# Optimization experiments

Hardware: AMD Instinct MI355X
Metric: run time of the kernel (lower is better)

Reference implementation:

```python
import jax, jax.numpy as jnp
import numpy as np

C = 512
NH = 4
HD = C // NH
G = 32  # min(32, C) and C % 32 == 0
EPS = 1e-5


def setup_inputs() -> dict:
    key = jax.random.key(0)
    ks = jax.random.split(key, 11)
    s = 1.0 / np.sqrt(C)
    return {
        "x": jax.random.normal(ks[0], (16, C, 32, 32), dtype=jnp.float32),
        "gamma": jnp.ones((C,), jnp.float32),
        "beta": jnp.zeros((C,), jnp.float32),
        "wq": jax.random.normal(ks[1], (C, C), jnp.float32) * s,
        "bq": jax.random.normal(ks[2], (C,), jnp.float32) * 0.01,
        "wk": jax.random.normal(ks[3], (C, C), jnp.float32) * s,
        "bk": jax.random.normal(ks[4], (C,), jnp.float32) * 0.01,
        "wv": jax.random.normal(ks[5], (C, C), jnp.float32) * s,
        "bv": jax.random.normal(ks[6], (C,), jnp.float32) * 0.01,
        "wp": jax.random.normal(ks[7], (C, C), jnp.float32) * s,
        "bp": jax.random.normal(ks[8], (C,), jnp.float32) * 0.01,
    }


def _group_norm(x, gamma, beta):
    b, c, h, w = x.shape
    xr = x.reshape(b, G, c // G, h, w)
    mean = xr.mean(axis=(2, 3, 4), keepdims=True)
    var = xr.var(axis=(2, 3, 4), keepdims=True)
    xn = ((xr - mean) * jax.lax.rsqrt(var + EPS)).reshape(b, c, h, w)
    return xn * gamma[None, :, None, None] + beta[None, :, None, None]


def _conv1x1(x, w, b):
    # 1x1 conv == per-position channel GEMM
    return jnp.einsum('oc,bchw->bohw', w, x) + b[None, :, None, None]


def reference(x, gamma, beta, wq, bq, wk, bk, wv, bv, wp, bp):
    b, c, h, w = x.shape
    hw = h * w
    scale = HD ** (-0.5)
    hn = _group_norm(x, gamma, beta)
    q = _conv1x1(hn, wq, bq).reshape(b, NH, HD, hw)
    k = _conv1x1(hn, wk, bk).reshape(b, NH, HD, hw)
    v = _conv1x1(hn, wv, bv).reshape(b, NH, HD, hw)
    attn = jnp.einsum('bhdq,bhdk->bhqk', q, k) * scale  # [b, nh, hw, hw]
    attn = jax.nn.softmax(attn, axis=-1)
    out = jnp.einsum('bhqk,bhdk->bhdq', attn, v)  # [b, nh, hd, hw]
    out = out.reshape(b, c, h, w)
    out = _conv1x1(out, wp, bp)
    return x + out
```

## Files before the change

kernel.cpp:

```cpp
#include <hip/hip_runtime.h>
#include <math.h>

#define CCH 512
#define NH 4
#define HD 128
#define HW 1024
#define BATCH 16
#define EPS 1e-5f

typedef __attribute__((ext_vector_type(8))) short bfrag;
typedef __attribute__((ext_vector_type(4))) float f4;
typedef __attribute__((ext_vector_type(16))) float f16v;

static __device__ __forceinline__ unsigned short f2bf(float f) {
  union { float f; unsigned u; } v;
  v.f = f;
  unsigned r = v.u + 0x7fff + ((v.u >> 16) & 1);
  return (unsigned short)(r >> 16);
}
static __device__ __forceinline__ unsigned pack2(unsigned short a, unsigned short b) {
  return (unsigned)a | ((unsigned)b << 16);
}
static __device__ __forceinline__ unsigned cvt_pk_bf16(float a, float b) {
  unsigned r;
  asm("v_cvt_pk_bf16_f32 %0, %1, %2" : "=v"(r) : "v"(a), "v"(b));
  return r;
}
#if defined(__has_builtin) && __has_builtin(__builtin_amdgcn_exp2f)
#define EXP2(x) __builtin_amdgcn_exp2f(x)
#else
#define EXP2(x) __expf((x) * 0.6931471805599453f)
#endif
static __device__ __forceinline__ void ldg_lds16(const unsigned short* g,
                                                 unsigned short* l) {
  __builtin_amdgcn_global_load_lds(
      (const __attribute__((address_space(1))) unsigned int*)g,
      (__attribute__((address_space(3))) unsigned int*)l, 16, 0, 0);
}

#define QSCALE (0.08838834764831845f * 1.4426950408889634f)

__global__ __launch_bounds__(256) void wcvt_kernel(const float* __restrict__ s0,
                                                   const float* __restrict__ s1,
                                                   const float* __restrict__ s2,
                                                   const float* __restrict__ s3,
                                                   unsigned short* __restrict__ d) {
  const float* srcs[4] = {s0, s1, s2, s3};
  const float* s = srcs[blockIdx.y];
  unsigned short* dp = d + (size_t)blockIdx.y * CCH * CCH;
  int i = blockIdx.x * 256 + threadIdx.x;
  f4 v = ((const f4*)s)[i];
  ushort4 o;
  o.x = f2bf(v.x); o.y = f2bf(v.y); o.z = f2bf(v.z); o.w = f2bf(v.w);
  ((ushort4*)dp)[i] = o;
}

__global__ __launch_bounds__(256) void gn_kernel(const float* __restrict__ x,
                                                 const float* __restrict__ gamma,
                                                 const float* __restrict__ beta,
                                                 unsigned short* __restrict__ hn) {
  int b = blockIdx.x >> 5, g = blockIdx.x & 31;
  const float* xp = x + ((size_t)b * CCH + g * 16) * HW;
  int t = threadIdx.x;
  float s = 0.f, ss = 0.f;
  const f4* xp4 = (const f4*)xp;
  f4 vv[16];
#pragma unroll
  for (int c = 0; c < 16; ++c) {
    f4 v = xp4[c * 256 + t];
    vv[c] = v;
    s += v.x + v.y + v.z + v.w;
    ss += v.x * v.x + v.y * v.y + v.z * v.z + v.w * v.w;
  }
#pragma unroll
  for (int off = 32; off > 0; off >>= 1) {
    s += __shfl_xor(s, off);
    ss += __shfl_xor(ss, off);
  }
  __shared__ float rs[4], rss[4];
  int w = t >> 6;
  if ((t & 63) == 0) { rs[w] = s; rss[w] = ss; }
  __syncthreads();
  s = rs[0] + rs[1] + rs[2] + rs[3];
  ss = rss[0] + rss[1] + rss[2] + rss[3];
  const float invn = 1.f / (16 * HW);
  float mean = s * invn;
  float var = ss * invn - mean * mean;
  float rstd = rsqrtf(var + EPS);
  float a_[16], b_[16];
#pragma unroll
  for (int c = 0; c < 16; ++c) {
    float gm = gamma[g * 16 + c] * rstd;
    a_[c] = gm;
    b_[c] = beta[g * 16 + c] - mean * gm;
  }
#pragma unroll
  for (int i = 0; i < 4; ++i) {
    int p = 4 * t + i;
    uint4 u0, u1;
    u0.x = cvt_pk_bf16(vv[0][i] * a_[0] + b_[0], vv[1][i] * a_[1] + b_[1]);
    u0.y = cvt_pk_bf16(vv[2][i] * a_[2] + b_[2], vv[3][i] * a_[3] + b_[3]);
    u0.z = cvt_pk_bf16(vv[4][i] * a_[4] + b_[4], vv[5][i] * a_[5] + b_[5]);
    u0.w = cvt_pk_bf16(vv[6][i] * a_[6] + b_[6], vv[7][i] * a_[7] + b_[7]);
    u1.x = cvt_pk_bf16(vv[8][i] * a_[8] + b_[8], vv[9][i] * a_[9] + b_[9]);
    u1.y = cvt_pk_bf16(vv[10][i] * a_[10] + b_[10], vv[11][i] * a_[11] + b_[11]);
    u1.z = cvt_pk_bf16(vv[12][i] * a_[12] + b_[12], vv[13][i] * a_[13] + b_[13]);
    u1.w = cvt_pk_bf16(vv[14][i] * a_[14] + b_[14], vv[15][i] * a_[15] + b_[15]);
    unsigned short* dst = hn + ((size_t)b * HW + p) * CCH + g * 16;
    *(uint4*)dst = u0;
    *(uint4*)(dst + 8) = u1;
  }
}

template <int PROJ>
__global__ __launch_bounds__(256, 3) void mm_kernel(
    const unsigned short* __restrict__ Xt, const unsigned short* __restrict__ Wb,
    const float* __restrict__ b0, const float* __restrict__ b1,
    const float* __restrict__ b2, const float* __restrict__ resid,
    unsigned short* __restrict__ O0, unsigned short* __restrict__ O1,
    unsigned short* __restrict__ O2, float* __restrict__ Ofp) {
  int b = blockIdx.z;
  int p0 = blockIdx.x * 128;
  int c0g = blockIdx.y * 128;
  __shared__ __align__(16) unsigned short Xs[2][4096];
  __shared__ __align__(16) unsigned short Ws[2][4096];
  int t = threadIdx.x;
  int w = t >> 6, lane = t & 63, l15 = lane & 15, quad = lane >> 4;
  int wp = (w & 1) * 64, wc = (w >> 1) * 64;
  const unsigned short* Xb = Xt + (size_t)b * HW * CCH;
  const unsigned short* Wr = Wb + (size_t)c0g * CCH;
  f4 acc[4][4] = {};
  auto stage = [&](int k0, int bi) {
#pragma unroll
    for (int j = 0; j < 2; ++j) {
      int chk = w * 2 + j;
      int r = chk * 16 + (lane >> 2);
      int c = (lane & 3) ^ (r & 3);
      ldg_lds16(&Xb[(size_t)(p0 + r) * CCH + k0 + c * 8], &Xs[bi][chk * 512]);
      ldg_lds16(&Wr[(size_t)r * CCH + k0 + c * 8], &Ws[bi][chk * 512]);
    }
  };
  stage(0, 0);
  __syncthreads();
  for (int k0 = 0, cur = 0; k0 < CCH; k0 += 32, cur ^= 1) {
    if (k0 + 32 < CCH) stage(k0 + 32, cur ^ 1);
    bfrag af[4], bf[4];
#pragma unroll
    for (int pt = 0; pt < 4; ++pt) {
      int r = wp + pt * 16 + l15;
      af[pt] = *(const bfrag*)&Xs[cur][r * 32 + (quad ^ (r & 3)) * 8];
    }
#pragma unroll
    for (int ct = 0; ct < 4; ++ct) {
      int r = wc + ct * 16 + l15;
      bf[ct] = *(const bfrag*)&Ws[cur][r * 32 + (quad ^ (r & 3)) * 8];
    }
#pragma unroll
    for (int pt = 0; pt < 4; ++pt)
#pragma unroll
      for (int ct = 0; ct < 4; ++ct)
        acc[pt][ct] = __builtin_amdgcn_mfma_f32_16x16x32_bf16(
            af[pt], bf[ct], acc[pt][ct], 0, 0, 0);
    __syncthreads();
  }
  if (PROJ) {
#pragma unroll
    for (int ct = 0; ct < 4; ++ct) {
      int ch = c0g + wc + ct * 16 + l15;
      float bi = b0[ch];
#pragma unroll
      for (int pt = 0; pt < 4; ++pt) {
        int pos = p0 + wp + pt * 16 + quad * 4;
        f4 v = acc[pt][ct];
        size_t off = (size_t)b * CCH * HW + (size_t)ch * HW + pos;
        float4 rv = *(const float4*)&resid[off];
        float4 st;
        st.x = v.x + bi + rv.x; st.y = v.y + bi + rv.y;
        st.z = v.z + bi + rv.z; st.w = v.w + bi + rv.w;
        *(float4*)&Ofp[off] = st;
      }
    }
  } else {
    int mat = c0g >> 9;
    int c0 = c0g & 511;
    const float* bias = mat == 0 ? b0 : (mat == 1 ? b1 : b2);
    unsigned short* O = mat == 0 ? O0 : (mat == 1 ? O1 : O2);
    const float sc = (mat == 0) ? QSCALE : 1.0f;
#pragma unroll
    for (int ct = 0; ct < 4; ++ct) {
      int ch = c0 + wc + ct * 16 + l15;
      float bi = bias[ch];
#pragma unroll
      for (int pt = 0; pt < 4; ++pt) {
        int pos = p0 + wp + pt * 16 + quad * 4;
        f4 v = acc[pt][ct];
        if (mat < 2) {
          unsigned short* Op = O + (size_t)b * HW * CCH;
          Op[(size_t)(pos + 0) * CCH + ch] = f2bf((v.x + bi) * sc);
          Op[(size_t)(pos + 1) * CCH + ch] = f2bf((v.y + bi) * sc);
          Op[(size_t)(pos + 2) * CCH + ch] = f2bf((v.z + bi) * sc);
          Op[(size_t)(pos + 3) * CCH + ch] = f2bf((v.w + bi) * sc);
        } else {
          unsigned short* Op = O + (size_t)b * CCH * HW;
          ushort4 st;
          st.x = f2bf(v.x + bi); st.y = f2bf(v.y + bi);
          st.z = f2bf(v.z + bi); st.w = f2bf(v.w + bi);
          *(ushort4*)&Op[(size_t)ch * HW + pos] = st;
        }
      }
    }
  }
}

__global__ __launch_bounds__(256, 2) void attn_kernel(
    const unsigned short* __restrict__ Qt, const unsigned short* __restrict__ Kt,
    const unsigned short* __restrict__ Vc, unsigned short* __restrict__ Ot) {
  int bh = blockIdx.x;
  int b = bh >> 2, h = bh & 3;
  int q0 = blockIdx.y * 128;
  int t = threadIdx.x;
  int w = t >> 6, lane = t & 63;
  int l31 = lane & 31, half = lane >> 5;
  __shared__ __align__(16) unsigned short Ks[2][64 * 128];
  __shared__ __align__(16) unsigned short Vs[2][128 * 64];
  int q = q0 + w * 32 + l31;
  const unsigned short* Kbase = Kt + (size_t)b * HW * CCH + h * HD;
  const unsigned short* Vbase = Vc + ((size_t)b * CCH + h * HD) * HW;
  bfrag qf[8];
#pragma unroll
  for (int ks = 0; ks < 8; ++ks)
    qf[ks] = *(const bfrag*)&Qt[((size_t)b * HW + q) * CCH + h * HD +
                                ks * 16 + half * 8];
  f16v o[4] = {};
  float ls[4] = {};
  auto stage = [&](int kt, int bi) {
    int kk0 = kt * 64;
#pragma unroll
    for (int j = 0; j < 4; ++j) {
      int chk = w * 4 + j;
      {
        int r = chk * 4 + (lane >> 4);
        int c = (lane & 15) ^ (r & 15);
        ldg_lds16(&Kbase[(size_t)(kk0 + r) * CCH + c * 8], &Ks[bi][chk * 512]);
      }
      {
        int r = chk * 8 + (lane >> 3);
        int c = (lane & 7) ^ (r & 7);
        ldg_lds16(&Vbase[(size_t)r * HW + kk0 + c * 8], &Vs[bi][chk * 512]);
      }
    }
  };
  stage(0, 0);
  for (int kt = 0; kt < 16; ++kt) {
    __syncthreads();
    if (kt < 15) stage(kt + 1, (kt + 1) & 1);
    const unsigned short* K_ = Ks[kt & 1];
    const unsigned short* V_ = Vs[kt & 1];
    f16v S[2] = {};
    __builtin_amdgcn_s_setprio(1);
#pragma unroll
    for (int ks = 0; ks < 8; ++ks) {
      int c16 = ks * 2 + half;
#pragma unroll
      for (int mt = 0; mt < 2; ++mt) {
        int r = mt * 32 + l31;
        bfrag kf = *(const bfrag*)&K_[r * 128 + ((c16 ^ (r & 15)) << 3)];
        S[mt] = __builtin_amdgcn_mfma_f32_32x32x16_bf16(kf, qf[ks], S[mt],
                                                        0, 0, 0);
      }
    }
    __builtin_amdgcn_s_setprio(0);
    unsigned pd[16];
#pragma unroll
    for (int mt = 0; mt < 2; ++mt)
#pragma unroll
      for (int i = 0; i < 8; ++i) {
        float p0 = EXP2(S[mt][2 * i]);
        float p1 = EXP2(S[mt][2 * i + 1]);
        ls[i & 3] += p0 + p1;
        pd[mt * 8 + i] = cvt_pk_bf16(p0, p1);
      }
#pragma unroll
    for (int mt = 0; mt < 2; ++mt)
#pragma unroll
      for (int s = 0; s < 2; ++s) {
        int base = mt * 8 + s * 4;
        unsigned a0 = pd[base + 0], a1 = pd[base + 1];
        unsigned c0 = pd[base + 2], c1 = pd[base + 3];
        asm("v_permlane32_swap_b32 %0, %1" : "+v"(a0), "+v"(c0));
        asm("v_permlane32_swap_b32 %0, %1" : "+v"(a1), "+v"(c1));
        union { unsigned u[4]; bfrag f; } pf;
        pf.u[0] = a0; pf.u[1] = a1; pf.u[2] = c0; pf.u[3] = c1;
        int c8 = (mt * 2 + s) * 2 + half;
        __builtin_amdgcn_s_setprio(1);
#pragma unroll
        for (int dt = 0; dt < 4; ++dt) {
          int r = dt * 32 + l31;
          bfrag vf = *(const bfrag*)&V_[r * 64 + ((c8 ^ (r & 7)) << 3)];
          o[dt] = __builtin_amdgcn_mfma_f32_32x32x16_bf16(vf, pf.f, o[dt],
                                                          0, 0, 0);
        }
        __builtin_amdgcn_s_setprio(0);
      }
  }
  float lrow = (ls[0] + ls[1]) + (ls[2] + ls[3]);
  lrow += __shfl_xor(lrow, 32);
  float inv = 1.f / lrow;
  unsigned short* Op = Ot + ((size_t)b * HW + q) * CCH + h * HD;
#pragma unroll
  for (int dt = 0; dt < 4; ++dt)
#pragma unroll
    for (int rg = 0; rg < 4; ++rg) {
      int d = dt * 32 + rg * 8 + half * 4;
      uint2 st;
      st.x = cvt_pk_bf16(o[dt][rg * 4 + 0] * inv, o[dt][rg * 4 + 1] * inv);
      st.y = cvt_pk_bf16(o[dt][rg * 4 + 2] * inv, o[dt][rg * 4 + 3] * inv);
      *(uint2*)&Op[d] = st;
    }
}

extern "C" void kernel_launch(void* const* d_in, const int* in_sizes, int n_in,
                              void* d_out, int out_size, void* d_ws,
                              size_t ws_size, hipStream_t stream) {
  const float* x = (const float*)d_in[0];
  const float* gamma = (const float*)d_in[1];
  const float* beta = (const float*)d_in[2];
  const float* wq = (const float*)d_in[3];
  const float* bq = (const float*)d_in[4];
  const float* wk = (const float*)d_in[5];
  const float* bk = (const float*)d_in[6];
  const float* wv = (const float*)d_in[7];
  const float* bv = (const float*)d_in[8];
  const float* wp = (const float*)d_in[9];
  const float* bp = (const float*)d_in[10];

  const size_t TS = (size_t)BATCH * HW * CCH;
  unsigned short* wB = (unsigned short*)d_ws;
  unsigned short* hn = wB + (size_t)4 * CCH * CCH;
  unsigned short* Qt = hn + TS;
  unsigned short* Kt = Qt + TS;
  unsigned short* Vc = Kt + TS;
  unsigned short* Ot = hn;

  wcvt_kernel<<<dim3(256, 4), 256, 0, stream>>>(wq, wk, wv, wp, wB);
  gn_kernel<<<dim3(BATCH * 32), 256, 0, stream>>>(x, gamma, beta, hn);
  mm_kernel<0><<<dim3(8, 12, BATCH), 256, 0, stream>>>(
      hn, wB, bq, bk, bv, nullptr, Qt, Kt, Vc, nullptr);
  attn_kernel<<<dim3(64, 8), 256, 0, stream>>>(Qt, Kt, Vc, Ot);
  mm_kernel<1><<<dim3(8, 4, BATCH), 256, 0, stream>>>(
      Ot, wB + (size_t)3 * CCH * CCH, bp, bp, bp, x, nullptr, nullptr, nullptr,
      (float*)d_out);
}
```

Measured before the change: 211.4 us.

## Stage Q/K projection epilogue through LDS for coalesced row-major bf16 stores

For Q and K, the projection kernel now swaps the MFMA operands so each lane holds four consecutive channels. It writes the bf16 results into a swizzled LDS tile and then stores whole rows with 16-byte coalesced writes, replacing the old scattered 2-byte stores with a large stride. V moves to its own launch (MODE 1) with packed-convert stores, and the LDS swizzle for the K-tile loads changes to reduce bank conflicts. The cost is an extra launch and an additional LDS pass plus barrier in the epilogue.

```diff
diff --git a/kernel.cpp b/kernel.cpp
--- a/kernel.cpp
+++ b/kernel.cpp
@@ -17,9 +17,6 @@
   v.f = f;
   unsigned r = v.u + 0x7fff + ((v.u >> 16) & 1);
   return (unsigned short)(r >> 16);
-}
-static __device__ __forceinline__ unsigned pack2(unsigned short a, unsigned short b) {
-  return (unsigned)a | ((unsigned)b << 16);
 }
 static __device__ __forceinline__ unsigned cvt_pk_bf16(float a, float b) {
   unsigned r;
@@ -39,6 +36,8 @@
 }
 
 #define QSCALE (0.08838834764831845f * 1.4426950408889634f)
+
+#define SWZ(r) (((r) ^ ((r) >> 2)) & 3)
 
 __global__ __launch_bounds__(256) void wcvt_kernel(const float* __restrict__ s0,
                                                    const float* __restrict__ s1,
@@ -112,18 +111,19 @@
   }
 }
 
-template <int PROJ>
+template <int MODE>
 __global__ __launch_bounds__(256, 3) void mm_kernel(
     const unsigned short* __restrict__ Xt, const unsigned short* __restrict__ Wb,
     const float* __restrict__ b0, const float* __restrict__ b1,
-    const float* __restrict__ b2, const float* __restrict__ resid,
+    const float* __restrict__ resid,
     unsigned short* __restrict__ O0, unsigned short* __restrict__ O1,
-    unsigned short* __restrict__ O2, float* __restrict__ Ofp) {
+    float* __restrict__ Ofp) {
   int b = blockIdx.z;
   int p0 = blockIdx.x * 128;
   int c0g = blockIdx.y * 128;
-  __shared__ __align__(16) unsigned short Xs[2][4096];
-  __shared__ __align__(16) unsigned short Ws[2][4096];
+  __shared__ __align__(16) unsigned short LDS[16384];
+#define XS(bi) (LDS + (bi) * 4096)
+#define WS(bi) (LDS + 8192 + (bi) * 4096)
   int t = threadIdx.x;
   int w = t >> 6, lane = t & 63, l15 = lane & 15, quad = lane >> 4;
   int wp = (w & 1) * 64, wc = (w >> 1) * 64;
@@ -135,9 +135,9 @@
     for (int j = 0; j < 2; ++j) {
       int chk = w * 2 + j;
       int r = chk * 16 + (lane >> 2);
-      int c = (lane & 3) ^ (r & 3);
-      ldg_lds16(&Xb[(size_t)(p0 + r) * CCH + k0 + c * 8], &Xs[bi][chk * 512]);
-      ldg_lds16(&Wr[(size_t)r * CCH + k0 + c * 8], &Ws[bi][chk * 512]);
+      int c = (lane & 3) ^ SWZ(r);
+      ldg_lds16(&Xb[(size_t)(p0 + r) * CCH + k0 + c * 8], XS(bi) + chk * 512);
+      ldg_lds16(&Wr[(size_t)r * CCH + k0 + c * 8], WS(bi) + chk * 512);
     }
   };
   stage(0, 0);
@@ -148,22 +148,73 @@
 #pragma unroll
     for (int pt = 0; pt < 4; ++pt) {
       int r = wp + pt * 16 + l15;
-      af[pt] = *(const bfrag*)&Xs[cur][r * 32 + (quad ^ (r & 3)) * 8];
+      af[pt] = *(const bfrag*)&XS(cur)[r * 32 + ((quad ^ SWZ(r)) << 3)];
     }
 #pragma unroll
     for (int ct = 0; ct < 4; ++ct) {
       int r = wc + ct * 16 + l15;
-      bf[ct] = *(const bfrag*)&Ws[cur][r * 32 + (quad ^ (r & 3)) * 8];
+      bf[ct] = *(const bfrag*)&WS(cur)[r * 32 + ((quad ^ SWZ(r)) << 3)];
     }
 #pragma unroll
     for (int pt = 0; pt < 4; ++pt)
 #pragma unroll
-      for (int ct = 0; ct < 4; ++ct)
-        acc[pt][ct] = __builtin_amdgcn_mfma_f32_16x16x32_bf16(
-            af[pt], bf[ct], acc[pt][ct], 0, 0, 0);
+      for (int ct = 0; ct < 4; ++ct) {
+        if (MODE == 0)
+          acc[pt][ct] = __builtin_amdgcn_mfma_f32_16x16x32_bf16(
+              bf[ct], af[pt], acc[pt][ct], 0, 0, 0);
+        else
+          acc[pt][ct] = __builtin_amdgcn_mfma_f32_16x16x32_bf16(
+              af[pt], bf[ct], acc[pt][ct], 0, 0, 0);
+      }
     __syncthreads();
   }
-  if (PROJ) {
+  if (MODE == 0) {
+    int mat = c0g >> 9;
+    int c0 = c0g & 511;
+    const float* bias = mat ? b1 : b0;
+    unsigned short* O = mat ? O1 : O0;
+    const float sc = mat ? 1.0f : QSCALE;
+#pragma unroll
+    for (int ct = 0; ct < 4; ++ct) {
+      f4 bi = *(const f4*)&bias[c0 + wc + ct * 16 + quad * 4];
+      int g = (wc >> 2) + ct * 4 + quad;
+#pragma unroll
+      for (int pt = 0; pt < 4; ++pt) {
+        int pos = wp + pt * 16 + l15;
+        f4 v = acc[pt][ct];
+        uint2 d;
+        d.x = cvt_pk_bf16((v.x + bi.x) * sc, (v.y + bi.y) * sc);
+        d.y = cvt_pk_bf16((v.z + bi.z) * sc, (v.w + bi.w) * sc);
+        int gs = g ^ ((pos & 7) << 1);
+        *(uint2*)&LDS[pos * 128 + gs * 4] = d;
+      }
+    }
+    __syncthreads();
+    unsigned short* Op = O + (size_t)b * HW * CCH;
+#pragma unroll
+    for (int it = 0; it < 8; ++it) {
+      int row = w * 32 + it * 4 + (lane >> 4);
+      int g0 = (2 * l15) ^ ((row & 7) << 1);
+      uint4 val = *(const uint4*)&LDS[row * 128 + g0 * 4];
+      *(uint4*)&Op[(size_t)(p0 + row) * CCH + c0 + l15 * 8] = val;
+    }
+  } else if (MODE == 1) {
+#pragma unroll
+    for (int ct = 0; ct < 4; ++ct) {
+      int ch = c0g + wc + ct * 16 + l15;
+      float bi = b0[ch];
+      unsigned short* Op = O0 + (size_t)b * CCH * HW;
+#pragma unroll
+      for (int pt = 0; pt < 4; ++pt) {
+        int pos = p0 + wp + pt * 16 + quad * 4;
+        f4 v = acc[pt][ct];
+        uint2 st;
+        st.x = cvt_pk_bf16(v.x + bi, v.y + bi);
+        st.y = cvt_pk_bf16(v.z + bi, v.w + bi);
+        *(uint2*)&Op[(size_t)ch * HW + pos] = st;
+      }
+    }
+  } else {
 #pragma unroll
     for (int ct = 0; ct < 4; ++ct) {
       int ch = c0g + wc + ct * 16 + l15;
@@ -180,36 +231,9 @@
         *(float4*)&Ofp[off] = st;
       }
     }
-  } else {
-    int mat = c0g >> 9;
-    int c0 = c0g & 511;
-    const float* bias = mat == 0 ? b0 : (mat == 1 ? b1 : b2);
-    unsigned short* O = mat == 0 ? O0 : (mat == 1 ? O1 : O2);
-    const float sc = (mat == 0) ? QSCALE : 1.0f;
-#pragma unroll
-    for (int ct = 0; ct < 4; ++ct) {
-      int ch = c0 + wc + ct * 16 + l15;
-      float bi = bias[ch];
-#pragma unroll
-      for (int pt = 0; pt < 4; ++pt) {
-        int pos = p0 + wp + pt * 16 + quad * 4;
-        f4 v = acc[pt][ct];
-        if (mat < 2) {
-          unsigned short* Op = O + (size_t)b * HW * CCH;
-          Op[(size_t)(pos + 0) * CCH + ch] = f2bf((v.x + bi) * sc);
-          Op[(size_t)(pos + 1) * CCH + ch] = f2bf((v.y + bi) * sc);
-          Op[(size_t)(pos + 2) * CCH + ch] = f2bf((v.z + bi) * sc);
-          Op[(size_t)(pos + 3) * CCH + ch] = f2bf((v.w + bi) * sc);
-        } else {
-          unsigned short* Op = O + (size_t)b * CCH * HW;
-          ushort4 st;
-          st.x = f2bf(v.x + bi); st.y = f2bf(v.y + bi);
-          st.z = f2bf(v.z + bi); st.w = f2bf(v.w + bi);
-          *(ushort4*)&Op[(size_t)ch * HW + pos] = st;
-        }
-      }
-    }
-  }
+  }
+#undef XS
+#undef WS
 }
 
 __global__ __launch_bounds__(256, 2) void attn_kernel(
@@ -344,10 +368,13 @@
 
   wcvt_kernel<<<dim3(256, 4), 256, 0, stream>>>(wq, wk, wv, wp, wB);
   gn_kernel<<<dim3(BATCH * 32), 256, 0, stream>>>(x, gamma, beta, hn);
-  mm_kernel<0><<<dim3(8, 12, BATCH), 256, 0, stream>>>(
-      hn, wB, bq, bk, bv, nullptr, Qt, Kt, Vc, nullptr);
+  mm_kernel<0><<<dim3(8, 8, BATCH), 256, 0, stream>>>(
+      hn, wB, bq, bk, nullptr, Qt, Kt, nullptr);
+  mm_kernel<1><<<dim3(8, 4, BATCH), 256, 0, stream>>>(
+      hn, wB + (size_t)2 * CCH * CCH, bv, nullptr, nullptr, Vc, nullptr,
+      nullptr);
   attn_kernel<<<dim3(64, 8), 256, 0, stream>>>(Qt, Kt, Vc, Ot);
-  mm_kernel<1><<<dim3(8, 4, BATCH), 256, 0, stream>>>(
-      Ot, wB + (size_t)3 * CCH * CCH, bp, bp, bp, x, nullptr, nullptr, nullptr,
+  mm_kernel<2><<<dim3(8, 4, BATCH), 256, 0, stream>>>(
+      Ot, wB + (size_t)3 * CCH * CCH, bp, nullptr, x, nullptr, nullptr,
       (float*)d_out);
 }
```

After: 206.3 us. 2.4% less time.
